# Kernel optimization log

Measured on AMD Instinct MI355X. Metric: run time of the kernel, lower is better.

## Reference

```python
import jax, jax.numpy as jnp
import numpy as np

B, C, H, W = 32, 512, 64, 64
RED = 16  # reduction -> hidden = C // RED = 32


def setup_inputs() -> dict:
    key = jax.random.key(0)
    k1, k2, k3 = jax.random.split(key, 3)
    hid = C // RED
    x = jax.random.normal(k1, (B, C, H, W), dtype=jnp.float32)
    # torch Linear(in, out, bias=False) weight shape [out, in]
    w1 = jax.random.normal(k2, (hid, C), dtype=jnp.float32) * (1.0 / np.sqrt(C))
    w2 = jax.random.normal(k3, (C, hid), dtype=jnp.float32) * (1.0 / np.sqrt(hid))
    return {"x": x, "w1": w1, "w2": w2}


def reference(x, w1, w2):
    # global average pool over H,W -> (B, C)
    v = jnp.mean(x, axis=(2, 3))
    # squeeze-excite MLP: C -> C//r -> C
    h = jax.nn.relu(jnp.einsum('bc,hc->bh', v, w1))
    g = jax.nn.sigmoid(jnp.einsum('bh,ch->bc', h, w2))
    # broadcast channel-wise scale
    return x * g[:, :, None, None]
```

## Files before the change

### kernel.cpp

```cpp
#include <hip/hip_runtime.h>
#include <stdint.h>

#define BB 32
#define CC 512
#define HW 4096
#define HID 32

__global__ __launch_bounds__(256) void se_pool(const float* __restrict__ x,
                                               float* __restrict__ v) {
    const int bc = blockIdx.x;
    const float4* __restrict__ p4 = (const float4*)(x + (size_t)bc * HW);
    const int t = threadIdx.x;

    float s = 0.f;
#pragma unroll
    for (int it = 0; it < 4; ++it) {
        float4 d = p4[it * 256 + t];
        s += d.x + d.y + d.z + d.w;
    }
#pragma unroll
    for (int off = 32; off > 0; off >>= 1) s += __shfl_down(s, off, 64);

    __shared__ float ws[4];
    const int lane = t & 63, wid = t >> 6;
    if (lane == 0) ws[wid] = s;
    __syncthreads();
    if (t == 0) {
        float tot = ws[0] + ws[1] + ws[2] + ws[3];
        v[bc] = tot * (1.0f / (float)HW);
    }
}

__global__ __launch_bounds__(1024) void se_mlp(const float* __restrict__ v,
                                               const float* __restrict__ w1,
                                               const float* __restrict__ w2,
                                               float* __restrict__ g) {
    __shared__ float vs[BB * CC];
    __shared__ float h[BB * HID];
    const int t = threadIdx.x;

    for (int i = t; i < BB * CC; i += 1024) vs[i] = v[i];
    __syncthreads();

    {
        const int b = t >> 5, j = t & 31;
        const float* __restrict__ wr = w1 + j * CC;
        const float* __restrict__ vr = vs + b * CC;
        float s = 0.f;
        for (int c = 0; c < CC; ++c) s += vr[c] * wr[c];
        h[b * HID + j] = s > 0.f ? s : 0.f;
    }
    __syncthreads();

    for (int e = t; e < BB * CC; e += 1024) {
        const int b = e >> 9, c = e & (CC - 1);
        const float* __restrict__ wr = w2 + c * HID;
        const float* __restrict__ hr = h + b * HID;
        float s = 0.f;
#pragma unroll
        for (int j = 0; j < HID; ++j) s += hr[j] * wr[j];
        g[e] = 1.0f / (1.0f + __expf(-s));
    }
}

__global__ __launch_bounds__(256) void se_scale(const float* __restrict__ x,
                                                const float* __restrict__ g,
                                                float* __restrict__ out) {
    const int bc = blockIdx.x;
    const float gate = g[bc];
    const float4* __restrict__ xp = (const float4*)(x + (size_t)bc * HW);
    float4* __restrict__ op = (float4*)(out + (size_t)bc * HW);
    const int t = threadIdx.x;

#pragma unroll
    for (int it = 0; it < 4; ++it) {
        float4 d = xp[it * 256 + t];
        d.x *= gate; d.y *= gate; d.z *= gate; d.w *= gate;
        op[it * 256 + t] = d;
    }
}

extern "C" void kernel_launch(void* const* d_in, const int* in_sizes, int n_in,
                              void* d_out, int out_size, void* d_ws, size_t ws_size,
                              hipStream_t stream) {
    const float* x  = (const float*)d_in[0];
    const float* w1 = (const float*)d_in[1];
    const float* w2 = (const float*)d_in[2];
    float* out = (float*)d_out;

    float* v = (float*)d_ws;
    float* g = v + BB * CC;

    se_pool <<<BB * CC, 256, 0, stream>>>(x, v);
    se_mlp  <<<1, 1024, 0, stream>>>(v, w1, w2, g);
    se_scale<<<BB * CC, 256, 0, stream>>>(x, g, out);
}
```

Baseline: 592.1 us.

## Chunk batch into cache-sized slices so scale pass rereads x from cache

Splits the batch into four chunks of 8 images and runs pool, MLP and scale per chunk, so each chunk's 64 MB of x may still be in the large last-level cache when the scale kernel rereads it. The scale kernel walks planes in reverse to hit the most recently pooled data first and uses nontemporal stores so the output does not evict x. The MLP kernel is also vectorised, with split-K dot products and shuffle reductions. The cost is twelve launches instead of three and a serial single-block MLP inside each chunk.

```diff
diff --git a/kernel.cpp b/kernel.cpp
--- a/kernel.cpp
+++ b/kernel.cpp
@@ -5,17 +5,23 @@
 #define CC 512
 #define HW 4096
 #define HID 32
+#define CB 8
+#define NCHUNK (BB / CB)
+#define PLANES_PER_CHUNK (CB * CC)
+
+typedef float f4 __attribute__((ext_vector_type(4)));
 
 __global__ __launch_bounds__(256) void se_pool(const float* __restrict__ x,
-                                               float* __restrict__ v) {
-    const int bc = blockIdx.x;
-    const float4* __restrict__ p4 = (const float4*)(x + (size_t)bc * HW);
+                                               float* __restrict__ v,
+                                               int plane0) {
+    const int plane = plane0 + blockIdx.x;
+    const f4* __restrict__ p4 = (const f4*)(x + (size_t)plane * HW);
     const int t = threadIdx.x;
 
     float s = 0.f;
 #pragma unroll
     for (int it = 0; it < 4; ++it) {
-        float4 d = p4[it * 256 + t];
+        f4 d = p4[it * 256 + t];
         s += d.x + d.y + d.z + d.w;
     }
 #pragma unroll
@@ -27,56 +33,68 @@
     __syncthreads();
     if (t == 0) {
         float tot = ws[0] + ws[1] + ws[2] + ws[3];
-        v[bc] = tot * (1.0f / (float)HW);
+        v[plane] = tot * (1.0f / (float)HW);
     }
 }
 
 __global__ __launch_bounds__(1024) void se_mlp(const float* __restrict__ v,
                                                const float* __restrict__ w1,
                                                const float* __restrict__ w2,
-                                               float* __restrict__ g) {
-    __shared__ float vs[BB * CC];
-    __shared__ float h[BB * HID];
+                                               float* __restrict__ g,
+                                               int b0) {
+    __shared__ float vs[CB * CC];
+    __shared__ float h[CB * HID];
     const int t = threadIdx.x;
 
-    for (int i = t; i < BB * CC; i += 1024) vs[i] = v[i];
+    for (int i = t; i < CB * CC; i += 1024) vs[i] = v[b0 * CC + i];
     __syncthreads();
 
     {
-        const int b = t >> 5, j = t & 31;
-        const float* __restrict__ wr = w1 + j * CC;
-        const float* __restrict__ vr = vs + b * CC;
+        const int dot = t >> 2, sub = t & 3;
+        const int b = dot >> 5, j = dot & (HID - 1);
+        const f4* __restrict__ wr = (const f4*)(w1 + j * CC) + sub * 32;
+        const f4* __restrict__ vr = (const f4*)(vs + b * CC) + sub * 32;
         float s = 0.f;
-        for (int c = 0; c < CC; ++c) s += vr[c] * wr[c];
-        h[b * HID + j] = s > 0.f ? s : 0.f;
+#pragma unroll
+        for (int i = 0; i < 32; ++i) {
+            f4 a = vr[i], w = wr[i];
+            s += a.x * w.x + a.y * w.y + a.z * w.z + a.w * w.w;
+        }
+        s += __shfl_xor(s, 1, 64);
+        s += __shfl_xor(s, 2, 64);
+        if (sub == 0) h[dot] = s > 0.f ? s : 0.f;
     }
     __syncthreads();
 
-    for (int e = t; e < BB * CC; e += 1024) {
+    for (int e = t; e < CB * CC; e += 1024) {
         const int b = e >> 9, c = e & (CC - 1);
-        const float* __restrict__ wr = w2 + c * HID;
-        const float* __restrict__ hr = h + b * HID;
+        const f4* __restrict__ wr = (const f4*)(w2 + c * HID);
+        const f4* __restrict__ hr = (const f4*)(h + b * HID);
         float s = 0.f;
 #pragma unroll
-        for (int j = 0; j < HID; ++j) s += hr[j] * wr[j];
-        g[e] = 1.0f / (1.0f + __expf(-s));
+        for (int q = 0; q < HID / 4; ++q) {
+            f4 a = hr[q], w = wr[q];
+            s += a.x * w.x + a.y * w.y + a.z * w.z + a.w * w.w;
+        }
+        g[b0 * CC + e] = 1.0f / (1.0f + __expf(-s));
     }
 }
 
 __global__ __launch_bounds__(256) void se_scale(const float* __restrict__ x,
                                                 const float* __restrict__ g,
-                                                float* __restrict__ out) {
-    const int bc = blockIdx.x;
-    const float gate = g[bc];
-    const float4* __restrict__ xp = (const float4*)(x + (size_t)bc * HW);
-    float4* __restrict__ op = (float4*)(out + (size_t)bc * HW);
+                                                float* __restrict__ out,
+                                                int plane0) {
+    const int plane = plane0 + (PLANES_PER_CHUNK - 1 - (int)blockIdx.x);
+    const float gate = g[plane];
+    const f4* __restrict__ xp = (const f4*)(x + (size_t)plane * HW);
+    f4* __restrict__ op = (f4*)(out + (size_t)plane * HW);
     const int t = threadIdx.x;
 
 #pragma unroll
     for (int it = 0; it < 4; ++it) {
-        float4 d = xp[it * 256 + t];
+        f4 d = xp[it * 256 + t];
         d.x *= gate; d.y *= gate; d.z *= gate; d.w *= gate;
-        op[it * 256 + t] = d;
+        __builtin_nontemporal_store(d, &op[it * 256 + t]);
     }
 }
 
@@ -91,7 +109,11 @@
     float* v = (float*)d_ws;
     float* g = v + BB * CC;
 
-    se_pool <<<BB * CC, 256, 0, stream>>>(x, v);
-    se_mlp  <<<1, 1024, 0, stream>>>(v, w1, w2, g);
-    se_scale<<<BB * CC, 256, 0, stream>>>(x, g, out);
+    for (int k = 0; k < NCHUNK; ++k) {
+        const int b0 = k * CB;
+        const int plane0 = b0 * CC;
+        se_pool <<<PLANES_PER_CHUNK, 256, 0, stream>>>(x, v, plane0);
+        se_mlp  <<<1, 1024, 0, stream>>>(v, w1, w2, g, b0);
+        se_scale<<<PLANES_PER_CHUNK, 256, 0, stream>>>(x, g, out, plane0);
+    }
 }
```

New measurement: 599.5 us. About the same (+1.2%).
